# Kernel tuning notes

Measured on AMD Instinct MI355X. Metric: run time of the kernel, lower is better.

The kernel has to match this reference:

```python
import jax, jax.numpy as jnp
import numpy as np

NUM_CLASSES = 172
IGNORE_INDEX = 255
DICE_WEIGHT = 0.5
EPS = 1e-7


def setup_inputs() -> dict:
    key = jax.random.key(0)
    k1, k2 = jax.random.split(key)
    pred = jax.random.normal(k1, (4, NUM_CLASSES, 256, 256), dtype=jnp.float32)
    target = jax.random.randint(k2, (4, 256, 256), 0, NUM_CLASSES, dtype=jnp.int32)
    return {"pred": pred, "target": target}


def reference(pred, target):
    # pred: [B, C, H, W] logits; target: [B, H, W] int labels (255 = ignore)
    C = NUM_CLASSES
    logp = jax.nn.log_softmax(pred, axis=1)  # [B, C, H, W]

    # ---- cross entropy with ignore_index (mean over valid pixels) ----
    valid = target != IGNORE_INDEX  # [B, H, W]
    safe_tgt = jnp.where(valid, target, 0)
    nll = -jnp.take_along_axis(logp, safe_tgt[:, None].astype(jnp.int32), axis=1)[:, 0]  # [B, H, W]
    n_valid = jnp.sum(valid)
    ce = jnp.sum(jnp.where(valid, nll, 0.0)) / jnp.maximum(n_valid, 1).astype(pred.dtype)

    # ---- dice loss: vectorized over classes (replaces per-class python loop) ----
    p = jnp.exp(logp)  # softmax probs [B, C, H, W]
    # intersection[c] = sum over pixels with target==c of p[:, c] at those pixels
    gathered = jnp.take_along_axis(p, safe_tgt[:, None].astype(jnp.int32), axis=1)[:, 0]  # [B, H, W]
    seg_ids = target.ravel().astype(jnp.int32)  # ignore pixels land in bucket 255, discarded
    inter = jax.ops.segment_sum(gathered.ravel(), seg_ids, num_segments=256)[:C]  # [C]
    counts = jax.ops.segment_sum(jnp.ones_like(gathered.ravel()), seg_ids, num_segments=256)[:C]
    union = jnp.sum(p, axis=(0, 2, 3)) + counts  # [C]
    valid_c = union > 0
    dice_terms = jnp.where(valid_c, (2.0 * inter + EPS) / (union + EPS), 0.0)
    n_valid_c = jnp.sum(valid_c).astype(pred.dtype)
    dice = jnp.where(n_valid_c > 0, 1.0 - jnp.sum(dice_terms) / jnp.maximum(n_valid_c, 1.0), 0.0)

    return ce + DICE_WEIGHT * dice
```

## Files before the change

kernel.cpp:

```cpp
#include <hip/hip_runtime.h>
#include <stdint.h>

#define NCLS 172
#define IGN 255
#define HW 65536
#define NPIX 262144
#define EPSV 1e-7f
#define TP 128
#define NTHR 512
#define HCLS 86
#define HROWS 96
#define HSZ (HROWS * TP)
#define NSTAGE 32
#define SS 520

__device__ __forceinline__ void gl_lds16(const float* g, float* l) {
    __builtin_amdgcn_global_load_lds(
        (const __attribute__((address_space(1))) void*)g,
        (__attribute__((address_space(3))) void*)l, 16, 0, 0);
}

__global__ __launch_bounds__(NTHR, 4) void seg_fused(
    const float* __restrict__ pred, const int* __restrict__ tgt,
    float* __restrict__ part)
{
    __shared__ float tile[HSZ];
    __shared__ float sPart[4 * TP];
    __shared__ int   sTgt[TP];
    __shared__ float sInter[NCLS];
    __shared__ float sUnion[NCLS];
    __shared__ unsigned int sCnt[NCLS];
    __shared__ float sCE[2];

    const int tid   = threadIdx.x;
    const int lane  = tid & 63;
    const int wv    = tid >> 6;
    const int p     = tid & (TP - 1);
    const int chunk = tid >> 7;

    for (int i = tid; i < NCLS; i += NTHR) { sInter[i] = 0.f; sUnion[i] = 0.f; sCnt[i] = 0u; }
    if (tid < 2) sCE[tid] = 0.f;
    const int pix0 = blockIdx.x * TP;
    if (tid < TP) sTgt[tid] = tgt[pix0 + tid];

    const int b   = pix0 >> 16;
    const int hw0 = pix0 & (HW - 1);
    const float* gb = pred + (size_t)b * NCLS * HW + hw0;

    const int srow = lane >> 5;
    const int spo  = (lane & 31) << 2;

    auto stage = [&](int half) {
        const int coff = half * HCLS;
        #pragma unroll
        for (int k6 = 0; k6 < 6; ++k6) {
            const int ib = wv + 8 * k6;
            int c = coff + 2 * ib + srow;
            if (c > NCLS - 1) c = NCLS - 1;
            gl_lds16(gb + (size_t)c * HW + spo, &tile[ib * 256]);
        }
    };

    float e[43];
    float sAcc = 0.f;

    stage(0);
    __syncthreads();
    #pragma unroll
    for (int k = 0; k < 43; ++k) {
        const int c = chunk + 4 * k;
        if (c < HCLS) { e[k] = __expf(tile[c * TP + p]); sAcc += e[k]; }
        else          { e[k] = 0.f; }
    }
    __syncthreads();

    stage(1);
    __syncthreads();
    #pragma unroll
    for (int k = 0; k < 43; ++k) {
        const int c = chunk + 4 * k;
        if (c >= HCLS) { e[k] = __expf(tile[(c - HCLS) * TP + p]); sAcc += e[k]; }
    }
    sPart[chunk * TP + p] = sAcc;
    __syncthreads();

    const float s = (sPart[p] + sPart[TP + p]) + (sPart[2 * TP + p] + sPart[3 * TP + p]);
    const float invs = 1.0f / s;

    const int t = sTgt[p];
    const bool valid = (t != IGN);
    float nll = 0.f, nv = 0.f;
    if (valid && (t & 3) == chunk) {
        float pt = 0.f;
        #pragma unroll
        for (int k = 0; k < 43; ++k)
            if ((t >> 2) == k) pt = e[k];
        pt *= invs;
        nll = -__logf(pt); nv = 1.f;
        atomicAdd(&sInter[t], pt);
        atomicAdd(&sCnt[t], 1u);
    }
    #pragma unroll
    for (int off = 32; off > 0; off >>= 1) {
        nll += __shfl_down(nll, off, 64);
        nv  += __shfl_down(nv,  off, 64);
    }
    if (lane == 0 && nv != 0.f) { atomicAdd(&sCE[0], nll); atomicAdd(&sCE[1], nv); }

    #pragma unroll
    for (int k = 0; k < 43; ++k) {
        float v = e[k] * invs;
        #pragma unroll
        for (int m = 32; m > 0; m >>= 1) v += __shfl_xor(v, m, 64);
        if (lane == 0) atomicAdd(&sUnion[chunk + 4 * k], v);
    }
    __syncthreads();

    float* pb = part + (size_t)(blockIdx.x & (NSTAGE - 1)) * SS;
    if (tid < NCLS) {
        const float vi = sInter[tid];
        if (vi != 0.f) atomicAdd(&pb[tid], vi);
        const unsigned int ci = sCnt[tid];
        if (ci != 0u) atomicAdd(&pb[NCLS + tid], (float)ci);
        atomicAdd(&pb[344 + tid], sUnion[tid]);
    }
    if (tid == 0) { atomicAdd(&pb[516], sCE[0]); atomicAdd(&pb[517], sCE[1]); }
}

__global__ __launch_bounds__(256) void seg_fin(
    const float* __restrict__ part, float* __restrict__ out)
{
    __shared__ float sT[256], sN[256];
    const int tid = threadIdx.x;
    float term = 0.f, nv = 0.f;
    if (tid < NCLS) {
        float inter = 0.f, cnt = 0.f, uni = 0.f;
        for (int st = 0; st < NSTAGE; ++st) {
            inter += part[st * SS + tid];
            cnt   += part[st * SS + NCLS + tid];
            uni   += part[st * SS + 344 + tid];
        }
        const float u = uni + cnt;
        if (u > 0.f) { term = (2.f * inter + EPSV) / (u + EPSV); nv = 1.f; }
    }
    sT[tid] = term; sN[tid] = nv;
    __syncthreads();
    #pragma unroll
    for (int s2 = 128; s2 > 0; s2 >>= 1) {
        if (tid < s2) { sT[tid] += sT[tid + s2]; sN[tid] += sN[tid + s2]; }
        __syncthreads();
    }
    if (tid == 0) {
        float ce = 0.f, nvl = 0.f;
        for (int st = 0; st < NSTAGE; ++st) {
            ce  += part[st * SS + 516];
            nvl += part[st * SS + 517];
        }
        const float ceo  = ce / fmaxf(nvl, 1.f);
        const float dice = (sN[0] > 0.f) ? (1.f - sT[0] / fmaxf(sN[0], 1.f)) : 0.f;
        out[0] = ceo + 0.5f * dice;
    }
}

extern "C" void kernel_launch(void* const* d_in, const int* in_sizes, int n_in,
                              void* d_out, int out_size, void* d_ws, size_t ws_size,
                              hipStream_t stream) {
    const float* pred = (const float*)d_in[0];
    const int*   tgt  = (const int*)d_in[1];
    float* out  = (float*)d_out;
    float* part = (float*)d_ws;

    hipMemsetAsync(d_ws, 0, NSTAGE * SS * sizeof(float), stream);
    seg_fused<<<NPIX / TP, NTHR, 0, stream>>>(pred, tgt, part);
    seg_fin<<<1, 256, 0, stream>>>(part, out);
}
```

Baseline: 282.0 us.

## Load logits directly from global into registers instead of staging through LDS

Replaces the two-phase global_load_lds staging of logits into a shared tile with direct coalesced per-thread global loads. Each of the four thread chunks now owns a contiguous block of 43 classes instead of interleaved classes. All loads can be in flight at once, and the LDS tile and its barriers go away. Occupancy is no longer pinned by launch bounds, and register pressure from 43 live loads may limit waves per SIMD.

```diff
diff --git a/kernel.cpp b/kernel.cpp
--- a/kernel.cpp
+++ b/kernel.cpp
@@ -8,25 +8,15 @@
 #define EPSV 1e-7f
 #define TP 128
 #define NTHR 512
-#define HCLS 86
-#define HROWS 96
-#define HSZ (HROWS * TP)
+#define CPC 43
 #define NSTAGE 32
 #define SS 520
 
-__device__ __forceinline__ void gl_lds16(const float* g, float* l) {
-    __builtin_amdgcn_global_load_lds(
-        (const __attribute__((address_space(1))) void*)g,
-        (__attribute__((address_space(3))) void*)l, 16, 0, 0);
-}
-
-__global__ __launch_bounds__(NTHR, 4) void seg_fused(
+__global__ __launch_bounds__(NTHR) void seg_fused(
     const float* __restrict__ pred, const int* __restrict__ tgt,
     float* __restrict__ part)
 {
-    __shared__ float tile[HSZ];
     __shared__ float sPart[4 * TP];
-    __shared__ int   sTgt[TP];
     __shared__ float sInter[NCLS];
     __shared__ float sUnion[NCLS];
     __shared__ unsigned int sCnt[NCLS];
@@ -34,68 +24,47 @@
 
     const int tid   = threadIdx.x;
     const int lane  = tid & 63;
-    const int wv    = tid >> 6;
     const int p     = tid & (TP - 1);
     const int chunk = tid >> 7;
+    const int c0    = chunk * CPC;
 
     for (int i = tid; i < NCLS; i += NTHR) { sInter[i] = 0.f; sUnion[i] = 0.f; sCnt[i] = 0u; }
     if (tid < 2) sCE[tid] = 0.f;
+
     const int pix0 = blockIdx.x * TP;
-    if (tid < TP) sTgt[tid] = tgt[pix0 + tid];
+    const int b    = pix0 >> 16;
+    const int hw0  = pix0 & (HW - 1);
+    const float* gp = pred + (size_t)b * NCLS * HW + (size_t)c0 * HW + hw0 + p;
 
-    const int b   = pix0 >> 16;
-    const int hw0 = pix0 & (HW - 1);
-    const float* gb = pred + (size_t)b * NCLS * HW + hw0;
-
-    const int srow = lane >> 5;
-    const int spo  = (lane & 31) << 2;
-
-    auto stage = [&](int half) {
-        const int coff = half * HCLS;
-        #pragma unroll
-        for (int k6 = 0; k6 < 6; ++k6) {
-            const int ib = wv + 8 * k6;
-            int c = coff + 2 * ib + srow;
-            if (c > NCLS - 1) c = NCLS - 1;
-            gl_lds16(gb + (size_t)c * HW + spo, &tile[ib * 256]);
-        }
-    };
-
-    float e[43];
-    float sAcc = 0.f;
-
-    stage(0);
-    __syncthreads();
+    float e[CPC];
+    float s0 = 0.f, s1 = 0.f, s2 = 0.f, s3 = 0.f;
     #pragma unroll
-    for (int k = 0; k < 43; ++k) {
-        const int c = chunk + 4 * k;
-        if (c < HCLS) { e[k] = __expf(tile[c * TP + p]); sAcc += e[k]; }
-        else          { e[k] = 0.f; }
+    for (int k = 0; k < 40; k += 4) {
+        e[k]     = __expf(gp[(size_t)(k    ) * HW]);
+        e[k + 1] = __expf(gp[(size_t)(k + 1) * HW]);
+        e[k + 2] = __expf(gp[(size_t)(k + 2) * HW]);
+        e[k + 3] = __expf(gp[(size_t)(k + 3) * HW]);
+        s0 += e[k]; s1 += e[k + 1]; s2 += e[k + 2]; s3 += e[k + 3];
     }
-    __syncthreads();
-
-    stage(1);
-    __syncthreads();
-    #pragma unroll
-    for (int k = 0; k < 43; ++k) {
-        const int c = chunk + 4 * k;
-        if (c >= HCLS) { e[k] = __expf(tile[(c - HCLS) * TP + p]); sAcc += e[k]; }
-    }
-    sPart[chunk * TP + p] = sAcc;
+    e[40] = __expf(gp[(size_t)40 * HW]); s0 += e[40];
+    e[41] = __expf(gp[(size_t)41 * HW]); s1 += e[41];
+    e[42] = __expf(gp[(size_t)42 * HW]); s2 += e[42];
+    sPart[chunk * TP + p] = (s0 + s1) + (s2 + s3);
     __syncthreads();
 
     const float s = (sPart[p] + sPart[TP + p]) + (sPart[2 * TP + p] + sPart[3 * TP + p]);
     const float invs = 1.0f / s;
 
-    const int t = sTgt[p];
+    const int t = tgt[pix0 + p];
     const bool valid = (t != IGN);
     float nll = 0.f, nv = 0.f;
-    if (valid && (t & 3) == chunk) {
-        float pt = 0.f;
+    if (valid && (t / CPC) == chunk) {
+        const int kt = t - chunk * CPC;
+        float et = 0.f;
         #pragma unroll
-        for (int k = 0; k < 43; ++k)
-            if ((t >> 2) == k) pt = e[k];
-        pt *= invs;
+        for (int k = 0; k < CPC; ++k)
+            if (kt == k) et = e[k];
+        const float pt = et * invs;
         nll = -__logf(pt); nv = 1.f;
         atomicAdd(&sInter[t], pt);
         atomicAdd(&sCnt[t], 1u);
@@ -108,11 +77,11 @@
     if (lane == 0 && nv != 0.f) { atomicAdd(&sCE[0], nll); atomicAdd(&sCE[1], nv); }
 
     #pragma unroll
-    for (int k = 0; k < 43; ++k) {
+    for (int k = 0; k < CPC; ++k) {
         float v = e[k] * invs;
         #pragma unroll
         for (int m = 32; m > 0; m >>= 1) v += __shfl_xor(v, m, 64);
-        if (lane == 0) atomicAdd(&sUnion[chunk + 4 * k], v);
+        if (lane == 0) atomicAdd(&sUnion[c0 + k], v);
     }
     __syncthreads();
 
```

Measured after the change: 268.5 us. -4.8%, faster.
